# Kernel optimization log

Measured on AMD Instinct MI355X. Metric: run time of the kernel, lower is better.

Reference implementation:

```python
import jax, jax.numpy as jnp
import numpy as np

F = 65536          # num_face
W_DIM = 512
PAD = 4096         # zero pad rows appended before gather
LRELU_SLOPE = 0.2
LRELU_GAIN = np.sqrt(2.0).astype(np.float32)  # def_gain of lrelu


def _fc(w, W, b):
    # StyleGAN FullyConnectedLayer: x @ W.T / sqrt(in_features) + bias
    gain = np.float32(1.0 / np.sqrt(W.shape[1]))
    return w @ W.T * gain + b


def _faceconv_gather(x, neigh, is_pad, k):
    # x: [B*F, C]; neigh/is_pad: [B*F, 9]; take first k neighbor slots.
    padded = jnp.concatenate([x, jnp.zeros((PAD, x.shape[1]), x.dtype)], axis=0)
    g = padded[neigh[:, :k]]                      # [B*F, k, C] irregular gather
    return jnp.where(is_pad[:, :k, None], jnp.zeros((), x.dtype), g)


def _modulated_face_conv(g, weight, styles, demodulate):
    # g: [B*F, k, I]; weight: [O, I, 1, k]; styles: [B, I]
    B = styles.shape[0]
    w = weight[None, :, :, 0, :] * styles[:, None, :, None]      # [B, O, I, k]
    if demodulate:
        d = jax.lax.rsqrt(jnp.sum(w * w, axis=(2, 3)) + 1e-8)    # [B, O]
        w = w * d[:, :, None, None]
    gb = g.reshape(B, -1, g.shape[1], g.shape[2])                # [B, F, k, I]
    out = jnp.einsum('bfki,boik->bfo', gb, w)                    # [B, F, O]
    return out.reshape(-1, w.shape[1])


def setup_inputs() -> dict:
    key = jax.random.key(0)
    ks = jax.random.split(key, 12)
    B = 2
    C = 128
    N = B * F
    face_neighborhood = jax.random.randint(ks[0], (N, 9), 0, N + PAD, dtype=jnp.int64)
    face_is_pad = jax.random.randint(ks[1], (N, 9), 0, 10) == 0
    return {
        'face_neighborhood': face_neighborhood,
        'face_is_pad': face_is_pad,
        'ws': jax.random.normal(ks[2], (B, 2, W_DIM), jnp.float32),
        'const': jax.random.normal(ks[3], (F, C), jnp.float32),
        'affine1_W': jax.random.normal(ks[4], (C, W_DIM), jnp.float32),
        'affine1_b': jnp.ones((C,), jnp.float32),
        'weight1': jax.random.normal(ks[5], (C, C, 1, 9), jnp.float32),
        'noise_const': jax.random.normal(ks[6], (F,), jnp.float32),
        'noise_strength': jnp.zeros((1,), jnp.float32),
        'bias1': jnp.zeros((C,), jnp.float32),
        'affine2_W': jax.random.normal(ks[7], (C, W_DIM), jnp.float32),
        'affine2_b': jnp.ones((C,), jnp.float32),
        'weight2': jax.random.normal(ks[8], (3, C, 1, 1), jnp.float32),
        'bias2': jnp.zeros((3,), jnp.float32),
    }


def reference(face_neighborhood, face_is_pad, ws, const, affine1_W, affine1_b,
              weight1, noise_const, noise_strength, bias1, affine2_W, affine2_b,
              weight2, bias2):
    # noise_mode == 'const'
    B = ws.shape[0]
    w0, w1 = ws[:, 0], ws[:, 1]
    x = jnp.tile(const[None], (B, 1, 1)).reshape(B * F, -1)        # [B*F, C]

    # --- SynthesisLayer conv1 ---
    styles = _fc(w0, affine1_W, affine1_b)                         # [B, C]
    noise = jnp.tile(noise_const[None], (B, 1)).reshape(-1, 1) * noise_strength
    g = _faceconv_gather(x, face_neighborhood, face_is_pad, 9)     # [B*F, 9, C]
    x = _modulated_face_conv(g, weight1, styles, demodulate=True)  # [B*F, C]
    x = x + noise
    x = jax.nn.leaky_relu(x + bias1[None, :], LRELU_SLOPE)
    x = jnp.clip(x * LRELU_GAIN, -256.0, 256.0)                    # clamp_gain

    # --- ToRGBLayer ---
    wg = np.float32(1.0 / np.sqrt(weight2.shape[1] * 1))
    styles2 = _fc(w1, affine2_W, affine2_b) * wg
    g2 = _faceconv_gather(x, face_neighborhood, face_is_pad, 1)    # [B*F, 1, C]
    img = _modulated_face_conv(g2, weight2, styles2, demodulate=False)
    img = jnp.clip(img + bias2[None, :], -256.0, 256.0)
    return x, img
```

## Files before the change

kernel.cpp:

```cpp
#include <hip/hip_runtime.h>

typedef unsigned short u16;
typedef __bf16 bf16x8 __attribute__((ext_vector_type(8)));
typedef float f32x4 __attribute__((ext_vector_type(4)));
typedef unsigned short u16x8 __attribute__((ext_vector_type(8)));

#define F_FACES 65536
#define N_FACES 131072
#define C_CH 128
#define WS_W2F 256
#define WS_S1 3328
#define WS_S2 4352
#define WS_W1 5376
#define WS_CONST 595200
#define XELEMS 16777216

__device__ inline u16 f2bf(float f) {
    unsigned u = __builtin_bit_cast(unsigned, f);
    unsigned r = (u + 0x7fffu + ((u >> 16) & 1u)) >> 16;
    return (u16)r;
}

__device__ inline void gl_lds16(const void* g, void* l) {
    __builtin_amdgcn_global_load_lds(
        (const __attribute__((address_space(1))) void*)g,
        (__attribute__((address_space(3))) void*)l, 16, 0, 0);
}

__global__ __launch_bounds__(256) void k0a_styles(
    const float* __restrict__ wsv, const float* __restrict__ a1W, const float* __restrict__ a1b,
    const float* __restrict__ a2W, const float* __restrict__ a2b, unsigned char* __restrict__ wsb)
{
    int wv = threadIdx.x >> 6, lane = threadIdx.x & 63;
    int c = blockIdx.x * 4 + wv;
    int which = c >> 8, rem = c & 255, b = rem >> 7, o = rem & 127;
    const float* W = (which ? a2W : a1W) + o * 512 + lane * 8;
    const float* x = wsv + (b * 2 + which) * 512 + lane * 8;
    float4 wa = *(const float4*)(W);
    float4 wb = *(const float4*)(W + 4);
    float4 xa = *(const float4*)(x);
    float4 xb = *(const float4*)(x + 4);
    float s = wa.x * xa.x + wa.y * xa.y + wa.z * xa.z + wa.w * xa.w
            + wb.x * xb.x + wb.y * xb.y + wb.z * xb.z + wb.w * xb.w;
#pragma unroll
    for (int d = 1; d < 64; d <<= 1) s += __shfl_xor(s, d);
    if (lane == 0) {
        const float g512 = 0.04419417382415922f;
        const float g128 = 0.08838834764831845f;
        float* wsf = (float*)wsb;
        if (which == 0) {
            wsf[WS_S1 / 4 + b * 128 + o] = s * g512 + a1b[o];
        } else {
            wsf[WS_S2 / 4 + b * 128 + o] = (s * g512 + a2b[o]) * g128;
        }
    }
}

__global__ __launch_bounds__(256) void k0f_fused(
    const float* __restrict__ cst, const float* __restrict__ w1g,
    const float* __restrict__ w2, unsigned char* __restrict__ wsb)
{
    __shared__ float red[4];
    int bid = blockIdx.x;
    int tid = threadIdx.x;

    if (bid >= 257) {
        u16* dst = (u16*)(wsb + WS_CONST);
        int base = ((bid - 257) * 256 + tid) * 8;
        float4 a = *(const float4*)(cst + base);
        float4 c = *(const float4*)(cst + base + 4);
        u16x8 p;
        p[0] = f2bf(a.x); p[1] = f2bf(a.y); p[2] = f2bf(a.z); p[3] = f2bf(a.w);
        p[4] = f2bf(c.x); p[5] = f2bf(c.y); p[6] = f2bf(c.z); p[7] = f2bf(c.w);
        *(u16x8*)(dst + base) = p;
        return;
    }
    if (bid < 256) {
        int bo = bid;
        int b = bo >> 7, o = bo & 127;
        const float* s1 = (const float*)(wsb + WS_S1) + b * 128;
        float sum = 0.f;
        for (int e = tid; e < 1152; e += 256) {
            int i = e / 9;
            float w = w1g[o * 1152 + e] * s1[i];
            sum += w * w;
        }
        int wv = tid >> 6, lane = tid & 63;
#pragma unroll
        for (int d = 1; d < 64; d <<= 1) sum += __shfl_xor(sum, d);
        if (lane == 0) red[wv] = sum;
        __syncthreads();
        float dm = rsqrtf(red[0] + red[1] + red[2] + red[3] + 1e-8f);
        u16* w1out = (u16*)(wsb + WS_W1);
        for (int wd = tid; wd < 576; wd += 256) {
            int k = wd >> 6;
            int ii = (wd & 63) * 2;
            float v0 = w1g[(o * 128 + ii) * 9 + k] * s1[ii] * dm;
            float v1 = w1g[(o * 128 + ii + 1) * 9 + k] * s1[ii + 1] * dm;
            unsigned pack = (unsigned)f2bf(v0) | ((unsigned)f2bf(v1) << 16);
            *(unsigned*)&w1out[(size_t)((((b * 9 + k) * 16 + (ii >> 3)) * 128 + o) * 8 + (ii & 7))] = pack;
        }
        return;
    }
    float* wsf = (float*)wsb;
    if (tid < 64) wsf[tid] = 0.f;
#pragma unroll
    for (int r = 0; r < 3; ++r) {
        int id = tid + r * 256;
        int b2 = id / 384;
        int rem = id - b2 * 384;
        int o2 = rem >> 7;
        int i = rem & 127;
        wsf[WS_W2F / 4 + id] = w2[o2 * 128 + i] * wsf[WS_S2 / 4 + b2 * 128 + i];
    }
}

__global__ __launch_bounds__(256, 5) void k1_conv(
    const int* __restrict__ neigh, const int* __restrict__ ispad,
    const float* __restrict__ noise_c, const float* __restrict__ nstr,
    const float* __restrict__ bias1, const unsigned char* __restrict__ wsb,
    float* __restrict__ out)
{
    __shared__ __align__(16) u16 As[2][64 * 128];

    const int tid = threadIdx.x;
    const int wv = tid >> 6, lane = tid & 63;
    const int quad = lane >> 4, l15 = lane & 15;
    const int f0 = blockIdx.x * 64;
    const int b = f0 >> 16;
    const u16* cst = (const u16*)(wsb + WS_CONST);
    const u16* w1ws = (const u16*)(wsb + WS_W1) + (size_t)b * 147456;
    const char* zp = (const char*)wsb;

    f32x4 acc[4][2] = {};
    int ia[4], ip[4];

#pragma unroll
    for (int r = 0; r < 4; ++r) {
        int nb = (f0 + (wv * 4 + r) * 4 + quad) * 9 + 0;
        ia[r] = neigh[nb]; ip[r] = ispad[nb];
    }
#pragma unroll
    for (int r = 0; r < 4; ++r) {
        int row = (wv * 4 + r) * 4 + quad;
        bool valid = (ip[r] == 0) && ((unsigned)ia[r] < 131072u);
        const char* src = valid ? (const char*)(cst + ((size_t)(ia[r] & 65535) << 7)) : zp;
        gl_lds16(src + ((l15 ^ (row & 15)) << 4), (char*)(&As[0][0]) + ((wv * 4 + r) << 10));
    }
#pragma unroll
    for (int r = 0; r < 4; ++r) {
        int nb = (f0 + (wv * 4 + r) * 4 + quad) * 9 + 1;
        ia[r] = neigh[nb]; ip[r] = ispad[nb];
    }

#pragma unroll
    for (int k = 0; k < 9; ++k) {
        bf16x8 bfr[4][2];
#pragma unroll
        for (int s = 0; s < 4; ++s)
#pragma unroll
            for (int nt = 0; nt < 2; ++nt)
                bfr[s][nt] = *reinterpret_cast<const bf16x8*>(
                    w1ws + (((k * 16 + s * 4 + quad) * 128) + wv * 32 + nt * 16 + l15) * 8);
        asm volatile("" ::: "memory");
        __builtin_amdgcn_sched_barrier(0);

        if (k < 8) {
#pragma unroll
            for (int r = 0; r < 4; ++r) {
                int row = (wv * 4 + r) * 4 + quad;
                bool valid = (ip[r] == 0) && ((unsigned)ia[r] < 131072u);
                const char* src = valid ? (const char*)(cst + ((size_t)(ia[r] & 65535) << 7)) : zp;
                gl_lds16(src + ((l15 ^ (row & 15)) << 4),
                         (char*)(&As[(k + 1) & 1][0]) + ((wv * 4 + r) << 10));
            }
        }
        if (k < 7) {
#pragma unroll
            for (int r = 0; r < 4; ++r) {
                int nb = (f0 + (wv * 4 + r) * 4 + quad) * 9 + (k + 2);
                ia[r] = neigh[nb]; ip[r] = ispad[nb];
            }
        }
        if (k < 7)       asm volatile("s_waitcnt vmcnt(20)" ::: "memory");
        else if (k == 7) asm volatile("s_waitcnt vmcnt(12)" ::: "memory");
        else             asm volatile("s_waitcnt vmcnt(8)" ::: "memory");
        __builtin_amdgcn_s_barrier();
        __builtin_amdgcn_sched_barrier(0);

        const u16* Ab = &As[k & 1][0];
#pragma unroll
        for (int s = 0; s < 4; ++s) {
            bf16x8 af[4];
#pragma unroll
            for (int mt = 0; mt < 4; ++mt) {
                int face = mt * 16 + l15;
                int chunk = (s * 4 + quad) ^ l15;
                af[mt] = *reinterpret_cast<const bf16x8*>(&Ab[face * 128 + chunk * 8]);
            }
#pragma unroll
            for (int mt = 0; mt < 4; ++mt)
#pragma unroll
                for (int nt = 0; nt < 2; ++nt)
                    acc[mt][nt] = __builtin_amdgcn_mfma_f32_16x16x32_bf16(
                        af[mt], bfr[s][nt], acc[mt][nt], 0, 0, 0);
        }
        asm volatile("s_waitcnt lgkmcnt(0)" ::: "memory");
        __builtin_amdgcn_s_barrier();
        __builtin_amdgcn_sched_barrier(0);
    }

    float ns = nstr[0];
    float b1v[2];
    b1v[0] = bias1[wv * 32 + l15];
    b1v[1] = bias1[wv * 32 + 16 + l15];
#pragma unroll
    for (int mt = 0; mt < 4; ++mt) {
#pragma unroll
        for (int r = 0; r < 4; ++r) {
            int face = f0 + mt * 16 + quad * 4 + r;
            float nz = noise_c[face & 65535] * ns;
#pragma unroll
            for (int nt = 0; nt < 2; ++nt) {
                float v = acc[mt][nt][r] + nz + b1v[nt];
                v = (v > 0.f) ? v : 0.2f * v;
                v *= 1.41421356f;
                v = fminf(fmaxf(v, -256.f), 256.f);
                out[(size_t)face * 128 + wv * 32 + nt * 16 + l15] = v;
            }
        }
    }
}

__global__ __launch_bounds__(256) void k2_img(
    const int* __restrict__ neigh, const int* __restrict__ ispad,
    const float* __restrict__ w2f, const float* __restrict__ bias2,
    const float* __restrict__ xbuf, float* __restrict__ imgout)
{
    __shared__ float ws2[768];
    int tid = threadIdx.x;
    ws2[tid] = w2f[tid];
    ws2[tid + 256] = w2f[tid + 256];
    ws2[tid + 512] = w2f[tid + 512];
    __syncthreads();
    int wv = tid >> 6, lane = tid & 63;
    int g = lane >> 4, sub = lane & 15;
    int face = blockIdx.x * 16 + wv * 4 + g;
    int b = face >> 16;
    int idx = neigh[face * 9];
    bool valid = (ispad[face * 9] == 0) && ((unsigned)idx < 131072u);
    float a0 = 0.f, a1 = 0.f, a2 = 0.f;
    if (valid) {
        float4 d0 = *(const float4*)(xbuf + (size_t)idx * 128 + sub * 8);
        float4 d1 = *(const float4*)(xbuf + (size_t)idx * 128 + sub * 8 + 4);
        float f[8] = {d0.x, d0.y, d0.z, d0.w, d1.x, d1.y, d1.z, d1.w};
        const float* w0 = &ws2[(b * 3 + 0) * 128 + sub * 8];
        const float* w1 = &ws2[(b * 3 + 1) * 128 + sub * 8];
        const float* w2p = &ws2[(b * 3 + 2) * 128 + sub * 8];
#pragma unroll
        for (int j = 0; j < 8; ++j) {
            a0 += f[j] * w0[j];
            a1 += f[j] * w1[j];
            a2 += f[j] * w2p[j];
        }
    }
#pragma unroll
    for (int d = 1; d < 16; d <<= 1) {
        a0 += __shfl_xor(a0, d);
        a1 += __shfl_xor(a1, d);
        a2 += __shfl_xor(a2, d);
    }
    if (sub < 3) {
        float v = (sub == 0) ? a0 : (sub == 1) ? a1 : a2;
        v += bias2[sub];
        v = fminf(fmaxf(v, -256.f), 256.f);
        imgout[face * 3 + sub] = v;
    }
}

extern "C" void kernel_launch(void* const* d_in, const int* in_sizes, int n_in,
                              void* d_out, int out_size, void* d_ws, size_t ws_size,
                              hipStream_t stream) {
    const int* neigh = (const int*)d_in[0];
    const int* ispad = (const int*)d_in[1];
    const float* wsv = (const float*)d_in[2];
    const float* cst = (const float*)d_in[3];
    const float* a1W = (const float*)d_in[4];
    const float* a1b = (const float*)d_in[5];
    const float* w1g = (const float*)d_in[6];
    const float* noise_c = (const float*)d_in[7];
    const float* nstr = (const float*)d_in[8];
    const float* bias1 = (const float*)d_in[9];
    const float* a2W = (const float*)d_in[10];
    const float* a2b = (const float*)d_in[11];
    const float* w2 = (const float*)d_in[12];
    const float* bias2 = (const float*)d_in[13];
    float* out = (float*)d_out;
    unsigned char* wsb = (unsigned char*)d_ws;

    k0a_styles<<<128, 256, 0, stream>>>(wsv, a1W, a1b, a2W, a2b, wsb);
    k0f_fused<<<4353, 256, 0, stream>>>(cst, w1g, w2, wsb);
    k1_conv<<<2048, 256, 0, stream>>>(neigh, ispad, noise_c, nstr, bias1, wsb, out);
    k2_img<<<8192, 256, 0, stream>>>(neigh, ispad, (const float*)(wsb + WS_W2F), bias2,
                                     out, out + XELEMS);
}
```

Measured before the change: 190.9 us.

## Fuse style affine into prep kernel, add nontemporal loads/stores, drop LDS staging in img

```diff
diff --git a/kernel.cpp b/kernel.cpp
--- a/kernel.cpp
+++ b/kernel.cpp
@@ -9,8 +9,6 @@
 #define N_FACES 131072
 #define C_CH 128
 #define WS_W2F 256
-#define WS_S1 3328
-#define WS_S2 4352
 #define WS_W1 5376
 #define WS_CONST 595200
 #define XELEMS 16777216
@@ -27,39 +25,18 @@
         (__attribute__((address_space(3))) void*)l, 16, 0, 0);
 }
 
-__global__ __launch_bounds__(256) void k0a_styles(
+__device__ inline f32x4 nt_load4(const float* p) {
+    return __builtin_nontemporal_load((const f32x4*)p);
+}
+
+__global__ __launch_bounds__(256) void k0_all(
     const float* __restrict__ wsv, const float* __restrict__ a1W, const float* __restrict__ a1b,
-    const float* __restrict__ a2W, const float* __restrict__ a2b, unsigned char* __restrict__ wsb)
-{
-    int wv = threadIdx.x >> 6, lane = threadIdx.x & 63;
-    int c = blockIdx.x * 4 + wv;
-    int which = c >> 8, rem = c & 255, b = rem >> 7, o = rem & 127;
-    const float* W = (which ? a2W : a1W) + o * 512 + lane * 8;
-    const float* x = wsv + (b * 2 + which) * 512 + lane * 8;
-    float4 wa = *(const float4*)(W);
-    float4 wb = *(const float4*)(W + 4);
-    float4 xa = *(const float4*)(x);
-    float4 xb = *(const float4*)(x + 4);
-    float s = wa.x * xa.x + wa.y * xa.y + wa.z * xa.z + wa.w * xa.w
-            + wb.x * xb.x + wb.y * xb.y + wb.z * xb.z + wb.w * xb.w;
-#pragma unroll
-    for (int d = 1; d < 64; d <<= 1) s += __shfl_xor(s, d);
-    if (lane == 0) {
-        const float g512 = 0.04419417382415922f;
-        const float g128 = 0.08838834764831845f;
-        float* wsf = (float*)wsb;
-        if (which == 0) {
-            wsf[WS_S1 / 4 + b * 128 + o] = s * g512 + a1b[o];
-        } else {
-            wsf[WS_S2 / 4 + b * 128 + o] = (s * g512 + a2b[o]) * g128;
-        }
-    }
-}
-
-__global__ __launch_bounds__(256) void k0f_fused(
+    const float* __restrict__ a2W, const float* __restrict__ a2b,
     const float* __restrict__ cst, const float* __restrict__ w1g,
     const float* __restrict__ w2, unsigned char* __restrict__ wsb)
 {
+    __shared__ float part[2][128];
+    __shared__ float s1sh[128];
     __shared__ float red[4];
     int bid = blockIdx.x;
     int tid = threadIdx.x;
@@ -67,22 +44,37 @@
     if (bid >= 257) {
         u16* dst = (u16*)(wsb + WS_CONST);
         int base = ((bid - 257) * 256 + tid) * 8;
-        float4 a = *(const float4*)(cst + base);
-        float4 c = *(const float4*)(cst + base + 4);
+        f32x4 a = nt_load4(cst + base);
+        f32x4 c = nt_load4(cst + base + 4);
         u16x8 p;
-        p[0] = f2bf(a.x); p[1] = f2bf(a.y); p[2] = f2bf(a.z); p[3] = f2bf(a.w);
-        p[4] = f2bf(c.x); p[5] = f2bf(c.y); p[6] = f2bf(c.z); p[7] = f2bf(c.w);
+        p[0] = f2bf(a[0]); p[1] = f2bf(a[1]); p[2] = f2bf(a[2]); p[3] = f2bf(a[3]);
+        p[4] = f2bf(c[0]); p[5] = f2bf(c[1]); p[6] = f2bf(c[2]); p[7] = f2bf(c[3]);
         *(u16x8*)(dst + base) = p;
         return;
     }
+    const float g512 = 0.04419417382415922f;
+    const float g128 = 0.08838834764831845f;
     if (bid < 256) {
-        int bo = bid;
-        int b = bo >> 7, o = bo & 127;
-        const float* s1 = (const float*)(wsb + WS_S1) + b * 128;
+        int b = bid >> 7, o = bid & 127;
+        int h = tid >> 7, i = tid & 127;
+        {
+            const float4* xr = (const float4*)(wsv + (size_t)(b * 2 + 0) * 512) + h * 64;
+            const float4* ar = (const float4*)(a1W + (size_t)i * 512) + h * 64;
+            float p = 0.f;
+#pragma unroll 8
+            for (int j = 0; j < 64; ++j) {
+                float4 w4 = ar[j], x4 = xr[j];
+                p += w4.x * x4.x + w4.y * x4.y + w4.z * x4.z + w4.w * x4.w;
+            }
+            part[h][i] = p;
+        }
+        __syncthreads();
+        if (tid < 128) s1sh[tid] = (part[0][tid] + part[1][tid]) * g512 + a1b[tid];
+        __syncthreads();
         float sum = 0.f;
         for (int e = tid; e < 1152; e += 256) {
-            int i = e / 9;
-            float w = w1g[o * 1152 + e] * s1[i];
+            int ii = e / 9;
+            float w = w1g[(size_t)o * 1152 + e] * s1sh[ii];
             sum += w * w;
         }
         int wv = tid >> 6, lane = tid & 63;
@@ -95,23 +87,37 @@
         for (int wd = tid; wd < 576; wd += 256) {
             int k = wd >> 6;
             int ii = (wd & 63) * 2;
-            float v0 = w1g[(o * 128 + ii) * 9 + k] * s1[ii] * dm;
-            float v1 = w1g[(o * 128 + ii + 1) * 9 + k] * s1[ii + 1] * dm;
+            float v0 = w1g[((size_t)o * 128 + ii) * 9 + k] * s1sh[ii] * dm;
+            float v1 = w1g[((size_t)o * 128 + ii + 1) * 9 + k] * s1sh[ii + 1] * dm;
             unsigned pack = (unsigned)f2bf(v0) | ((unsigned)f2bf(v1) << 16);
             *(unsigned*)&w1out[(size_t)((((b * 9 + k) * 16 + (ii >> 3)) * 128 + o) * 8 + (ii & 7))] = pack;
         }
         return;
     }
-    float* wsf = (float*)wsb;
-    if (tid < 64) wsf[tid] = 0.f;
-#pragma unroll
-    for (int r = 0; r < 3; ++r) {
-        int id = tid + r * 256;
-        int b2 = id / 384;
-        int rem = id - b2 * 384;
-        int o2 = rem >> 7;
-        int i = rem & 127;
-        wsf[WS_W2F / 4 + id] = w2[o2 * 128 + i] * wsf[WS_S2 / 4 + b2 * 128 + i];
+    {
+        float* s2sh = &part[0][0];
+        int b = tid >> 7, i = tid & 127;
+        const float4* xr = (const float4*)(wsv + (size_t)(b * 2 + 1) * 512);
+        const float4* ar = (const float4*)(a2W + (size_t)i * 512);
+        float p = 0.f;
+#pragma unroll 8
+        for (int j = 0; j < 128; ++j) {
+            float4 w4 = ar[j], x4 = xr[j];
+            p += w4.x * x4.x + w4.y * x4.y + w4.z * x4.z + w4.w * x4.w;
+        }
+        s2sh[tid] = (p * g512 + a2b[i]) * g128;
+        __syncthreads();
+        float* wsf = (float*)wsb;
+        if (tid < 64) wsf[tid] = 0.f;
+#pragma unroll
+        for (int r = 0; r < 3; ++r) {
+            int id = tid + r * 256;
+            int b2 = id / 384;
+            int rem = id - b2 * 384;
+            int o2 = rem >> 7;
+            int ii = rem & 127;
+            wsf[WS_W2F / 4 + id] = w2[o2 * 128 + ii] * s2sh[b2 * 128 + ii];
+        }
     }
 }
 
@@ -226,7 +232,7 @@
                 v = (v > 0.f) ? v : 0.2f * v;
                 v *= 1.41421356f;
                 v = fminf(fmaxf(v, -256.f), 256.f);
-                out[(size_t)face * 128 + wv * 32 + nt * 16 + l15] = v;
+                __builtin_nontemporal_store(v, &out[(size_t)face * 128 + wv * 32 + nt * 16 + l15]);
             }
         }
     }
@@ -237,12 +243,7 @@
     const float* __restrict__ w2f, const float* __restrict__ bias2,
     const float* __restrict__ xbuf, float* __restrict__ imgout)
 {
-    __shared__ float ws2[768];
     int tid = threadIdx.x;
-    ws2[tid] = w2f[tid];
-    ws2[tid + 256] = w2f[tid + 256];
-    ws2[tid + 512] = w2f[tid + 512];
-    __syncthreads();
     int wv = tid >> 6, lane = tid & 63;
     int g = lane >> 4, sub = lane & 15;
     int face = blockIdx.x * 16 + wv * 4 + g;
@@ -251,18 +252,21 @@
     bool valid = (ispad[face * 9] == 0) && ((unsigned)idx < 131072u);
     float a0 = 0.f, a1 = 0.f, a2 = 0.f;
     if (valid) {
-        float4 d0 = *(const float4*)(xbuf + (size_t)idx * 128 + sub * 8);
-        float4 d1 = *(const float4*)(xbuf + (size_t)idx * 128 + sub * 8 + 4);
-        float f[8] = {d0.x, d0.y, d0.z, d0.w, d1.x, d1.y, d1.z, d1.w};
-        const float* w0 = &ws2[(b * 3 + 0) * 128 + sub * 8];
-        const float* w1 = &ws2[(b * 3 + 1) * 128 + sub * 8];
-        const float* w2p = &ws2[(b * 3 + 2) * 128 + sub * 8];
-#pragma unroll
-        for (int j = 0; j < 8; ++j) {
-            a0 += f[j] * w0[j];
-            a1 += f[j] * w1[j];
-            a2 += f[j] * w2p[j];
-        }
+        const float* xr = xbuf + (size_t)idx * 128 + sub * 8;
+        f32x4 d0 = nt_load4(xr);
+        f32x4 d1 = nt_load4(xr + 4);
+        const float4* w04 = (const float4*)(w2f + (b * 3 + 0) * 128 + sub * 8);
+        const float4* w14 = (const float4*)(w2f + (b * 3 + 1) * 128 + sub * 8);
+        const float4* w24 = (const float4*)(w2f + (b * 3 + 2) * 128 + sub * 8);
+        float4 w0a = w04[0], w0b = w04[1];
+        float4 w1a = w14[0], w1b = w14[1];
+        float4 w2a = w24[0], w2b = w24[1];
+        a0 = d0[0] * w0a.x + d0[1] * w0a.y + d0[2] * w0a.z + d0[3] * w0a.w
+           + d1[0] * w0b.x + d1[1] * w0b.y + d1[2] * w0b.z + d1[3] * w0b.w;
+        a1 = d0[0] * w1a.x + d0[1] * w1a.y + d0[2] * w1a.z + d0[3] * w1a.w
+           + d1[0] * w1b.x + d1[1] * w1b.y + d1[2] * w1b.z + d1[3] * w1b.w;
+        a2 = d0[0] * w2a.x + d0[1] * w2a.y + d0[2] * w2a.z + d0[3] * w2a.w
+           + d1[0] * w2b.x + d1[1] * w2b.y + d1[2] * w2b.z + d1[3] * w2b.w;
     }
 #pragma unroll
     for (int d = 1; d < 16; d <<= 1) {
@@ -274,7 +278,7 @@
         float v = (sub == 0) ? a0 : (sub == 1) ? a1 : a2;
         v += bias2[sub];
         v = fminf(fmaxf(v, -256.f), 256.f);
-        imgout[face * 3 + sub] = v;
+        __builtin_nontemporal_store(v, &imgout[face * 3 + sub]);
     }
 }
 
@@ -298,8 +302,7 @@
     float* out = (float*)d_out;
     unsigned char* wsb = (unsigned char*)d_ws;
 
-    k0a_styles<<<128, 256, 0, stream>>>(wsv, a1W, a1b, a2W, a2b, wsb);
-    k0f_fused<<<4353, 256, 0, stream>>>(cst, w1g, w2, wsb);
+    k0_all<<<4353, 256, 0, stream>>>(wsv, a1W, a1b, a2W, a2b, cst, w1g, w2, wsb);
     k1_conv<<<2048, 256, 0, stream>>>(neigh, ispad, noise_c, nstr, bias1, wsb, out);
     k2_img<<<8192, 256, 0, stream>>>(neigh, ispad, (const float*)(wsb + WS_W2F), bias2,
                                      out, out + XELEMS);
```

New measurement: 228.4 us. 19.7% more time.
